# Kernel optimization log

Measured on AMD Instinct MI355X. Metric: run time of the kernel, lower is better.

The kernel has to match this reference:

```python
import jax, jax.numpy as jnp
import numpy as np

B, C, H, W = 32, 256, 64, 64
EPS = 1e-8  # clamp for cosine-similarity denominators


def setup_inputs() -> dict:
    key = jax.random.key(0)
    k1, k2, k3 = jax.random.split(key, 3)
    unmasked = jax.random.normal(k1, (B, C, H, W), dtype=jnp.float32)
    masked = jax.random.normal(k2, (B, C, H, W), dtype=jnp.float32)
    latent_mask = jax.random.randint(k3, (B, H, W), 0, 2, dtype=jnp.int32)
    return {
        "unmasked_latent_tensors": unmasked,
        "masked_latent_tensors": masked,
        "latent_mask": latent_mask,
    }


def reference(unmasked_latent_tensors, masked_latent_tensors, latent_mask):
    # Original torch code builds a full [B, B*H*W, H, W] cross-activation of a
    # cosine-similarity 1x1 conv (input vs. every masked position used as a
    # prototype), then gathers only the diagonal entries where batch index and
    # spatial position match. Mathematically that diagonal is just the
    # per-position cosine similarity along the channel axis, computed here
    # directly.
    u = unmasked_latent_tensors
    m = masked_latent_tensors
    num = jnp.sum(u * m, axis=1)                       # [B, H, W]
    u_norm = jnp.sqrt(jnp.sum(u * u, axis=1))          # [B, H, W]
    m_norm = jnp.sqrt(jnp.sum(m * m, axis=1))          # [B, H, W]
    sim = num / (jnp.maximum(u_norm, EPS) * jnp.maximum(m_norm, EPS))
    # masked=True: average similarity over mask==1 positions.
    mask_f = (latent_mask != 0).astype(sim.dtype)      # [B, H, W]
    return jnp.sum(sim * mask_f) / jnp.sum(mask_f)
```

## Files before the change

### kernel.cpp

```cpp
#include <hip/hip_runtime.h>


#define BB    32
#define CC    256
#define HH    64
#define WW    64
#define HWSZ  (HH * WW)
#define NPOS  (BB * HWSZ)
#define CSPLIT 16
#define CPER  (CC / CSPLIT)
#define PGPB  16
#define POSPB (PGPB * 4)
#define SIM_EPS 1e-8f

__global__ __launch_bounds__(256) void
sim_reduce_kernel(const float* __restrict__ u,
                  const float* __restrict__ m,
                  const int* __restrict__ mask,
                  double* __restrict__ ws)
{
    __shared__ float lds_num[CSPLIT * POSPB];
    __shared__ float lds_uu [CSPLIT * POSPB];
    __shared__ float lds_mm [CSPLIT * POSPB];

    const int tid    = threadIdx.x;
    const int posgrp = tid & (PGPB - 1);
    const int cchunk = tid >> 4;

    const int p0 = blockIdx.x * POSPB + posgrp * 4;
    const int b  = p0 >> 12;
    const int hw = p0 & (HWSZ - 1);

    const size_t base = (size_t)b * CC * HWSZ + (size_t)cchunk * CPER * HWSZ + hw;
    const float4* up = (const float4*)(u + base);
    const float4* mp = (const float4*)(m + base);

    float4 a[CPER], v[CPER];
#pragma unroll
    for (int c = 0; c < CPER; ++c) a[c] = up[(size_t)c * (HWSZ / 4)];
#pragma unroll
    for (int c = 0; c < CPER; ++c) v[c] = mp[(size_t)c * (HWSZ / 4)];

    float4 num = {0.f, 0.f, 0.f, 0.f};
    float4 uu  = {0.f, 0.f, 0.f, 0.f};
    float4 mm  = {0.f, 0.f, 0.f, 0.f};
#pragma unroll
    for (int c = 0; c < CPER; ++c) {
        num.x = fmaf(a[c].x, v[c].x, num.x); num.y = fmaf(a[c].y, v[c].y, num.y);
        num.z = fmaf(a[c].z, v[c].z, num.z); num.w = fmaf(a[c].w, v[c].w, num.w);
        uu.x  = fmaf(a[c].x, a[c].x, uu.x);  uu.y  = fmaf(a[c].y, a[c].y, uu.y);
        uu.z  = fmaf(a[c].z, a[c].z, uu.z);  uu.w  = fmaf(a[c].w, a[c].w, uu.w);
        mm.x  = fmaf(v[c].x, v[c].x, mm.x);  mm.y  = fmaf(v[c].y, v[c].y, mm.y);
        mm.z  = fmaf(v[c].z, v[c].z, mm.z);  mm.w  = fmaf(v[c].w, v[c].w, mm.w);
    }

    ((float4*)lds_num)[cchunk * PGPB + posgrp] = num;
    ((float4*)lds_uu )[cchunk * PGPB + posgrp] = uu;
    ((float4*)lds_mm )[cchunk * PGPB + posgrp] = mm;
    __syncthreads();

    if (tid < POSPB) {
        float n = 0.f, su = 0.f, sm = 0.f;
#pragma unroll
        for (int cc = 0; cc < CSPLIT; ++cc) {
            n  += lds_num[cc * POSPB + tid];
            su += lds_uu [cc * POSPB + tid];
            sm += lds_mm [cc * POSPB + tid];
        }
        const float denom = fmaxf(sqrtf(su), SIM_EPS) * fmaxf(sqrtf(sm), SIM_EPS);
        const float sim   = n / denom;
        const int   mk    = (mask[blockIdx.x * POSPB + tid] != 0) ? 1 : 0;
        double sd = mk ? (double)sim : 0.0;
        double md = (double)mk;
#pragma unroll
        for (int off = 32; off > 0; off >>= 1) {
            sd += __shfl_down(sd, off, 64);
            md += __shfl_down(md, off, 64);
        }
        if (tid == 0) {
            atomicAdd(&ws[0], sd);
            atomicAdd(&ws[1], md);
        }
    }
}

__global__ void finalize_kernel(const double* __restrict__ ws,
                                float* __restrict__ out)
{
    out[0] = (float)(ws[0] / ws[1]);
}

extern "C" void kernel_launch(void* const* d_in, const int* in_sizes, int n_in,
                              void* d_out, int out_size, void* d_ws, size_t ws_size,
                              hipStream_t stream)
{
    const float* u    = (const float*)d_in[0];
    const float* m    = (const float*)d_in[1];
    const int*   mask = (const int*)d_in[2];
    float*  out = (float*)d_out;
    double* ws  = (double*)d_ws;

    hipMemsetAsync(d_ws, 0, 2 * sizeof(double), stream);

    sim_reduce_kernel<<<NPOS / POSPB, 256, 0, stream>>>(u, m, mask, ws);
    finalize_kernel<<<1, 1, 0, stream>>>(ws, out);
}
```

Before: 282.9 us.

## Split cosine reduction into contiguous channel-slab pass and partial-combine pass

Replaces the single kernel, which read 16 strided channel rows per block, with two passes. The first pass has each block stream a contiguous 16-channel slab of one batch, 64KB per channel group, and write per-position partial dot products and squared norms to workspace. The second pass sums the 16 partials per position, applies the mask, and reduces through LDS, issuing one atomic per block instead of one per 64 positions. This gives more sequential DRAM access but adds about 25MB of partial writes and reads and an extra launch, and only 512 blocks run in pass one.

```diff
diff --git a/kernel.cpp b/kernel.cpp
--- a/kernel.cpp
+++ b/kernel.cpp
@@ -3,84 +3,110 @@
 
 #define BB    32
 #define CC    256
-#define HH    64
-#define WW    64
-#define HWSZ  (HH * WW)
+#define HWSZ  4096
 #define NPOS  (BB * HWSZ)
-#define CSPLIT 16
-#define CPER  (CC / CSPLIT)
-#define PGPB  16
-#define POSPB (PGPB * 4)
+#define G     16
+#define NCG   (CC / G)
 #define SIM_EPS 1e-8f
 
+#define WS_PARTIAL_OFF 256
+
 __global__ __launch_bounds__(256) void
-sim_reduce_kernel(const float* __restrict__ u,
-                  const float* __restrict__ m,
-                  const int* __restrict__ mask,
-                  double* __restrict__ ws)
+pass1_kernel(const float* __restrict__ u,
+             const float* __restrict__ m,
+             float* __restrict__ P)
 {
-    __shared__ float lds_num[CSPLIT * POSPB];
-    __shared__ float lds_uu [CSPLIT * POSPB];
-    __shared__ float lds_mm [CSPLIT * POSPB];
+    const int tid = threadIdx.x;
+    const int b   = blockIdx.x >> 4;
+    const int cg  = blockIdx.x & (NCG - 1);
 
-    const int tid    = threadIdx.x;
-    const int posgrp = tid & (PGPB - 1);
-    const int cchunk = tid >> 4;
+    const size_t slab = ((size_t)(b * CC + cg * G)) << 12;
+    const float4* up = (const float4*)(u + slab);
+    const float4* mp = (const float4*)(m + slab);
 
-    const int p0 = blockIdx.x * POSPB + posgrp * 4;
-    const int b  = p0 >> 12;
-    const int hw = p0 & (HWSZ - 1);
-
-    const size_t base = (size_t)b * CC * HWSZ + (size_t)cchunk * CPER * HWSZ + hw;
-    const float4* up = (const float4*)(u + base);
-    const float4* mp = (const float4*)(m + base);
-
-    float4 a[CPER], v[CPER];
+    float4 n[4], su[4], sm[4];
 #pragma unroll
-    for (int c = 0; c < CPER; ++c) a[c] = up[(size_t)c * (HWSZ / 4)];
-#pragma unroll
-    for (int c = 0; c < CPER; ++c) v[c] = mp[(size_t)c * (HWSZ / 4)];
-
-    float4 num = {0.f, 0.f, 0.f, 0.f};
-    float4 uu  = {0.f, 0.f, 0.f, 0.f};
-    float4 mm  = {0.f, 0.f, 0.f, 0.f};
-#pragma unroll
-    for (int c = 0; c < CPER; ++c) {
-        num.x = fmaf(a[c].x, v[c].x, num.x); num.y = fmaf(a[c].y, v[c].y, num.y);
-        num.z = fmaf(a[c].z, v[c].z, num.z); num.w = fmaf(a[c].w, v[c].w, num.w);
-        uu.x  = fmaf(a[c].x, a[c].x, uu.x);  uu.y  = fmaf(a[c].y, a[c].y, uu.y);
-        uu.z  = fmaf(a[c].z, a[c].z, uu.z);  uu.w  = fmaf(a[c].w, a[c].w, uu.w);
-        mm.x  = fmaf(v[c].x, v[c].x, mm.x);  mm.y  = fmaf(v[c].y, v[c].y, mm.y);
-        mm.z  = fmaf(v[c].z, v[c].z, mm.z);  mm.w  = fmaf(v[c].w, v[c].w, mm.w);
+    for (int g = 0; g < 4; ++g) {
+        n[g]  = make_float4(0.f, 0.f, 0.f, 0.f);
+        su[g] = make_float4(0.f, 0.f, 0.f, 0.f);
+        sm[g] = make_float4(0.f, 0.f, 0.f, 0.f);
     }
 
-    ((float4*)lds_num)[cchunk * PGPB + posgrp] = num;
-    ((float4*)lds_uu )[cchunk * PGPB + posgrp] = uu;
-    ((float4*)lds_mm )[cchunk * PGPB + posgrp] = mm;
+    for (int c = 0; c < G; ++c) {
+        const size_t cbase = (size_t)c * (HWSZ / 4);
+        float4 a[4], v[4];
+#pragma unroll
+        for (int g = 0; g < 4; ++g) a[g] = up[cbase + g * 256 + tid];
+#pragma unroll
+        for (int g = 0; g < 4; ++g) v[g] = mp[cbase + g * 256 + tid];
+#pragma unroll
+        for (int g = 0; g < 4; ++g) {
+            n[g].x  = fmaf(a[g].x, v[g].x, n[g].x);
+            n[g].y  = fmaf(a[g].y, v[g].y, n[g].y);
+            n[g].z  = fmaf(a[g].z, v[g].z, n[g].z);
+            n[g].w  = fmaf(a[g].w, v[g].w, n[g].w);
+            su[g].x = fmaf(a[g].x, a[g].x, su[g].x);
+            su[g].y = fmaf(a[g].y, a[g].y, su[g].y);
+            su[g].z = fmaf(a[g].z, a[g].z, su[g].z);
+            su[g].w = fmaf(a[g].w, a[g].w, su[g].w);
+            sm[g].x = fmaf(v[g].x, v[g].x, sm[g].x);
+            sm[g].y = fmaf(v[g].y, v[g].y, sm[g].y);
+            sm[g].z = fmaf(v[g].z, v[g].z, sm[g].z);
+            sm[g].w = fmaf(v[g].w, v[g].w, sm[g].w);
+        }
+    }
+
+    float4* P4 = (float4*)P;
+    const size_t pb = (size_t)(blockIdx.x * 3) * (HWSZ / 4);
+#pragma unroll
+    for (int g = 0; g < 4; ++g) {
+        P4[pb + 0 * (HWSZ / 4) + g * 256 + tid] = n[g];
+        P4[pb + 1 * (HWSZ / 4) + g * 256 + tid] = su[g];
+        P4[pb + 2 * (HWSZ / 4) + g * 256 + tid] = sm[g];
+    }
+}
+
+__global__ __launch_bounds__(256) void
+pass2_kernel(const float* __restrict__ P,
+             const int* __restrict__ mask,
+             double* __restrict__ ws)
+{
+    const int tid = threadIdx.x;
+    const int p   = blockIdx.x * 256 + tid;
+    const int b   = p >> 12;
+    const int hw  = p & (HWSZ - 1);
+
+    float n = 0.f, su = 0.f, sm = 0.f;
+#pragma unroll
+    for (int cg = 0; cg < NCG; ++cg) {
+        const size_t base = ((size_t)(b * NCG + cg) * 3) << 12;
+        n  += P[base + hw];
+        su += P[base + HWSZ + hw];
+        sm += P[base + 2 * HWSZ + hw];
+    }
+
+    const float denom = fmaxf(sqrtf(su), SIM_EPS) * fmaxf(sqrtf(sm), SIM_EPS);
+    const float sim   = n / denom;
+    const int   mk    = (mask[p] != 0) ? 1 : 0;
+    double sd = mk ? (double)sim : 0.0;
+    double md = (double)mk;
+
+#pragma unroll
+    for (int off = 32; off > 0; off >>= 1) {
+        sd += __shfl_down(sd, off, 64);
+        md += __shfl_down(md, off, 64);
+    }
+
+    __shared__ double red_s[4];
+    __shared__ double red_m[4];
+    const int wave = tid >> 6;
+    const int lane = tid & 63;
+    if (lane == 0) { red_s[wave] = sd; red_m[wave] = md; }
     __syncthreads();
 
-    if (tid < POSPB) {
-        float n = 0.f, su = 0.f, sm = 0.f;
-#pragma unroll
-        for (int cc = 0; cc < CSPLIT; ++cc) {
-            n  += lds_num[cc * POSPB + tid];
-            su += lds_uu [cc * POSPB + tid];
-            sm += lds_mm [cc * POSPB + tid];
-        }
-        const float denom = fmaxf(sqrtf(su), SIM_EPS) * fmaxf(sqrtf(sm), SIM_EPS);
-        const float sim   = n / denom;
-        const int   mk    = (mask[blockIdx.x * POSPB + tid] != 0) ? 1 : 0;
-        double sd = mk ? (double)sim : 0.0;
-        double md = (double)mk;
-#pragma unroll
-        for (int off = 32; off > 0; off >>= 1) {
-            sd += __shfl_down(sd, off, 64);
-            md += __shfl_down(md, off, 64);
-        }
-        if (tid == 0) {
-            atomicAdd(&ws[0], sd);
-            atomicAdd(&ws[1], md);
-        }
+    if (tid == 0) {
+        atomicAdd(&ws[0], red_s[0] + red_s[1] + red_s[2] + red_s[3]);
+        atomicAdd(&ws[1], red_m[0] + red_m[1] + red_m[2] + red_m[3]);
     }
 }
 
@@ -99,9 +125,11 @@
     const int*   mask = (const int*)d_in[2];
     float*  out = (float*)d_out;
     double* ws  = (double*)d_ws;
+    float*  P   = (float*)((char*)d_ws + WS_PARTIAL_OFF);
 
     hipMemsetAsync(d_ws, 0, 2 * sizeof(double), stream);
 
-    sim_reduce_kernel<<<NPOS / POSPB, 256, 0, stream>>>(u, m, mask, ws);
+    pass1_kernel<<<BB * NCG, 256, 0, stream>>>(u, m, P);
+    pass2_kernel<<<NPOS / 256, 256, 0, stream>>>(P, mask, ws);
     finalize_kernel<<<1, 1, 0, stream>>>(ws, out);
 }
```

New measurement: 299.4 us. 1.06x slower.
